# Kernel tuning notes

Hardware: AMD Instinct MI355X
Metric: run time of the kernel (lower is better)

The kernel has to match this reference:

```python
import jax, jax.numpy as jnp
import numpy as np

N_NODES = 20000
NUM_KERNELS = 2
K_DIFF = 10  # max_diffusion_step
IN_DIM = 128
HID = 128
COMB = IN_DIM + HID  # 256
N_EDGES = 640000


def setup_inputs() -> dict:
    key = jax.random.key(0)
    ks = jax.random.split(key, 6)
    inp = jax.random.normal(ks[0], (N_NODES, IN_DIM), dtype=jnp.float32)
    hidden = jax.random.normal(ks[1], (N_NODES, HID), dtype=jnp.float32)
    edge_index = jax.random.randint(ks[2], (NUM_KERNELS, 2, N_EDGES), 0, N_NODES, dtype=jnp.int32)
    # ~row-stochastic-ish weights (avg degree 32) to keep diffusion stable
    edge_weight = jax.random.uniform(ks[3], (NUM_KERNELS, N_EDGES), dtype=jnp.float32) * (1.0 / 32.0)
    num_matrices = NUM_KERNELS * K_DIFF + 1  # 21
    W = jax.random.normal(ks[4], (num_matrices * COMB, HID), dtype=jnp.float32) * (1.0 / np.sqrt(num_matrices * COMB))
    b = jnp.zeros((HID,), dtype=jnp.float32)
    return {"input": inp, "hidden": hidden, "edge_index": edge_index,
            "edge_weight": edge_weight, "W": W, "b": b}


def _gconv(x, edge_index, edge_weight, W, b):
    # x: (N, F). Diffusion (Chebyshev) over each sparse support, concat, project.
    n = x.shape[0]
    feats = [x]  # x_0 shared across kernels
    for k in range(NUM_KERNELS):
        src = edge_index[k, 0]
        dst = edge_index[k, 1]
        w = edge_weight[k][:, None]

        def spmm(v):  # (A v)[dst] = sum_e w_e * v[src_e]
            return jax.ops.segment_sum(v[src] * w, dst, num_segments=n)

        x0, x1 = x, spmm(x)
        feats.append(x1)
        for _ in range(2, K_DIFF + 1):
            x2 = 2.0 * spmm(x1) - x0
            feats.append(x2)
            x0, x1 = x1, x2
    h = jnp.concatenate(feats, axis=1)  # (N, (NUM_KERNELS*K+1)*F)
    return h @ W + b


def reference(input, hidden, edge_index, edge_weight, W, b):
    combined = jnp.concatenate([input, hidden], axis=1)  # (N, COMB)
    r = jax.nn.sigmoid(_gconv(combined, edge_index, edge_weight, W, b))
    u = jax.nn.sigmoid(_gconv(combined, edge_index, edge_weight, W, b))
    combined2 = jnp.concatenate([input, r * hidden], axis=1)
    C = jax.nn.sigmoid(_gconv(combined2, edge_index, edge_weight, W, b))  # activation=sigmoid (default)
    output = u * hidden + (1.0 - u) * C
    return output  # output == new hidden
```

## Files before the change

kernel.cpp:

```cpp
#include <hip/hip_runtime.h>

#define NN 20000
#define NK 2
#define FC 256
#define FH 128
#define NE 640000
#define NB 21

typedef short v8s __attribute__((ext_vector_type(8)));
typedef float v4f __attribute__((ext_vector_type(4)));
typedef unsigned int uint;
typedef uint v2u __attribute__((ext_vector_type(2)));

__device__ __forceinline__ float bf2f(unsigned short h) {
    union { uint u; float f; } v; v.u = ((uint)h) << 16; return v.f;
}
__device__ __forceinline__ unsigned short f2bf(float f) {
    union { float f; uint u; } v; v.f = f;
    uint r = v.u + 0x7FFF + ((v.u >> 16) & 1);
    return (unsigned short)(r >> 16);
}
__device__ __forceinline__ float bflo(uint v) {
    union { uint u; float f; } t; t.u = v << 16; return t.f;
}
__device__ __forceinline__ float bfhi(uint v) {
    union { uint u; float f; } t; t.u = v & 0xffff0000u; return t.f;
}


__global__ __launch_bounds__(256) void k_hist(const int* __restrict__ ei, int* __restrict__ cnt) {
    int wg = blockIdx.x;
    int xcd = wg & 7, chunk = wg >> 3;
    int k = xcd & 1, q = xcd >> 1;
    int e = chunk * 256 + threadIdx.x;
    int dst = ei[(size_t)k * 2 * NE + NE + e];
    if (dst >= q * 5000 && dst < q * 5000 + 5000)
        atomicAdd(&cnt[k * NN + dst], 1);
}

__global__ __launch_bounds__(1024) void k_scan(const int* __restrict__ cnt, int* __restrict__ rp) {
    int k = blockIdx.x;
    __shared__ int part[1024];
    int t = threadIdx.x;
    int loc[20];
    int s = 0;
    if (t < 1000) {
#pragma unroll
        for (int j = 0; j < 20; ++j) { loc[j] = cnt[k * NN + t * 20 + j]; s += loc[j]; }
    }
    part[t] = s;
    __syncthreads();
    for (int off = 1; off < 1024; off <<= 1) {
        int add = (t >= off) ? part[t - off] : 0;
        __syncthreads();
        part[t] += add;
        __syncthreads();
    }
    int excl = (t == 0) ? 0 : part[t - 1];
    if (t < 1000) {
        int run = excl;
#pragma unroll
        for (int j = 0; j < 20; ++j) { rp[k * (NN + 1) + t * 20 + j] = run; run += loc[j]; }
        if (t == 999) rp[k * (NN + 1) + NN] = run;
    }
}

__global__ __launch_bounds__(256) void k_fill(const int* __restrict__ ei, const float* __restrict__ ew,
                                              const int* __restrict__ rp, int* __restrict__ fcnt,
                                              int2* __restrict__ ep) {
    int wg = blockIdx.x;
    int xcd = wg & 7, chunk = wg >> 3;
    int k = xcd & 1, q = xcd >> 1;
    int e = chunk * 256 + threadIdx.x;
    int dst = ei[(size_t)k * 2 * NE + NE + e];
    if (dst >= q * 5000 && dst < q * 5000 + 5000) {
        int src = ei[(size_t)k * 2 * NE + e];
        int pos = rp[k * (NN + 1) + dst] + atomicAdd(&fcnt[k * NN + dst], 1);
        int2 pk; pk.x = src; pk.y = __float_as_int(ew[(size_t)k * NE + e]);
        ep[(size_t)k * NE + pos] = pk;
    }
}


__global__ __launch_bounds__(256) void k_comb(const float* __restrict__ in, const float* __restrict__ hid,
                                              unsigned short* __restrict__ comb) {
    int i = blockIdx.x * 256 + threadIdx.x;
    int r = i >> 6, c4 = i & 63;
    float4 v = (c4 < 32) ? ((const float4*)(in  + (size_t)r * FH))[c4]
                         : ((const float4*)(hid + (size_t)r * FH))[c4 - 32];
    ushort4 o; o.x = f2bf(v.x); o.y = f2bf(v.y); o.z = f2bf(v.z); o.w = f2bf(v.w);
    *(ushort4*)&comb[(size_t)r * FC + c4 * 4] = o;
}


__global__ __launch_bounds__(256) void k_wcvt(const float* __restrict__ W, unsigned short* __restrict__ Wt) {
    int i = blockIdx.x * 256 + threadIdx.x;
    int blk = i >> 15;
    int rem = i & 32767;
    int n = rem >> 8, kk = rem & 255;
    Wt[i] = f2bf(W[((size_t)blk * FC + kk) * FH + n]);
}


#define LDK 72

__global__ __launch_bounds__(256, 2) void k_gemm(const unsigned short* __restrict__ X,
        const unsigned short* __restrict__ Wt, unsigned short* __restrict__ outb,
        float* __restrict__ outf, int jstep) {
    __shared__ unsigned short Xs[64 * LDK];
    __shared__ unsigned short Ws[128 * LDK];
    int t = threadIdx.x;
    int w = t >> 6, l = t & 63;
    int l15 = l & 15, lg = l >> 4;
    int bm = blockIdx.x * 64;
    int blk = jstep + 10 * blockIdx.y;
    const unsigned short* Wb = Wt + (size_t)blk * FH * FC;
    v4f acc[4][2];
#pragma unroll
    for (int a = 0; a < 4; ++a)
#pragma unroll
        for (int b = 0; b < 2; ++b) acc[a][b] = (v4f){0.f, 0.f, 0.f, 0.f};

    for (int c = 0; c < 4; ++c) {
#pragma unroll
        for (int i = 0; i < 2; ++i) {
            int s = t + i * 256;
            int row = s >> 3, c8 = s & 7;
            int grow = bm + row; if (grow >= NN) grow = NN - 1;
            *(v8s*)&Xs[row * LDK + c8 * 8] = *(const v8s*)(X + (size_t)grow * FC + c * 64 + c8 * 8);
        }
#pragma unroll
        for (int i = 0; i < 4; ++i) {
            int s = t + i * 256;
            int n = s >> 3, k8 = s & 7;
            *(v8s*)&Ws[n * LDK + k8 * 8] = *(const v8s*)(Wb + (size_t)n * FC + c * 64 + k8 * 8);
        }
        __syncthreads();
#pragma unroll
        for (int ks2 = 0; ks2 < 2; ++ks2) {
            int ko = ks2 * 32 + lg * 8;
            v8s a[4], b[2];
#pragma unroll
            for (int mf = 0; mf < 4; ++mf) a[mf] = *(const v8s*)&Xs[(mf * 16 + l15) * LDK + ko];
#pragma unroll
            for (int nf = 0; nf < 2; ++nf) b[nf] = *(const v8s*)&Ws[(w * 32 + nf * 16 + l15) * LDK + ko];
#pragma unroll
            for (int mf = 0; mf < 4; ++mf)
#pragma unroll
                for (int nf = 0; nf < 2; ++nf)
                    acc[mf][nf] = __builtin_amdgcn_mfma_f32_16x16x32_bf16(a[mf], b[nf], acc[mf][nf], 0, 0, 0);
        }
        __syncthreads();
    }
    unsigned short* ob = outb ? outb + (size_t)blockIdx.y * NN * FH : (unsigned short*)0;
#pragma unroll
    for (int mf = 0; mf < 4; ++mf) {
        int grow0 = bm + mf * 16 + lg * 4;
#pragma unroll
        for (int nf = 0; nf < 2; ++nf) {
            int gcol = w * 32 + nf * 16 + l15;
#pragma unroll
            for (int r = 0; r < 4; ++r) {
                int grow = grow0 + r;
                if (grow < NN) {
                    if (outf) outf[(size_t)grow * FH + gcol] = acc[mf][nf][r];
                    else      ob[(size_t)grow * FH + gcol] = f2bf(acc[mf][nf][r]);
                }
            }
        }
    }
}


__global__ __launch_bounds__(256) void k_spmm(const int* __restrict__ rp, const int2* __restrict__ ep,
        const v2u* __restrict__ b1, const v2u* __restrict__ b2,
        const v2u* __restrict__ y, v2u* __restrict__ outp, int mode) {
    int wg = blockIdx.x;
    int xcd = wg & 7, slot = wg >> 3;
    int k = (xcd >= 4) ? 1 : 0;
    int unit = (xcd & 3) * 1250 + slot;
    int lane = threadIdx.x & 63;
    int l31 = lane & 31, hl = lane >> 5;
    int row = unit * 4 + (threadIdx.x >> 6);
    int beg = rp[k * (NN + 1) + row], end = rp[k * (NN + 1) + row + 1];
    const v2u* __restrict__ gb = b1 + (size_t)k * NN * 32;
    const long long* epk = (const long long*)(ep + (size_t)k * NE);

    float a0 = 0.f, a1 = 0.f, a2 = 0.f, a3 = 0.f;

    for (int e0 = beg; e0 < end; e0 += 64) {
        int idx = e0 + lane;
        long long mye = (idx < end) ? __builtin_nontemporal_load(epk + idx) : 0ll;
        int mx = (int)mye;
        int my = (int)(mye >> 32);
        int cnt = min(64, end - e0);
        int j = 0;
        for (; j < cnt; j += 16) {
            v2u v[8]; float wv[8];
#pragma unroll
            for (int p = 0; p < 8; ++p) {
                int sA = __builtin_amdgcn_readlane(mx, j + 2 * p);
                int sB = __builtin_amdgcn_readlane(mx, j + 2 * p + 1);
                int s = hl ? sB : sA;
                v[p] = gb[(size_t)s * 32 + l31];
                int wA = __builtin_amdgcn_readlane(my, j + 2 * p);
                int wB = __builtin_amdgcn_readlane(my, j + 2 * p + 1);
                wv[p] = __int_as_float(hl ? wB : wA);
            }
#pragma unroll
            for (int p = 0; p < 8; ++p) {
                a0 += wv[p] * bflo(v[p].x); a1 += wv[p] * bfhi(v[p].x);
                a2 += wv[p] * bflo(v[p].y); a3 += wv[p] * bfhi(v[p].y);
            }
        }
    }
    a0 += __shfl_xor(a0, 32);
    a1 += __shfl_xor(a1, 32);
    a2 += __shfl_xor(a2, 32);
    a3 += __shfl_xor(a3, 32);

    if (hl == 0) {
        size_t o = (size_t)(k * NN + row) * 32 + l31;
        float r0, r1, r2, r3;
        if (mode == 0) {
            v2u yv = __builtin_nontemporal_load(y + o);
            r0 = bflo(yv.x) + 2.f * a0; r1 = bfhi(yv.x) + 2.f * a1;
            r2 = bflo(yv.y) + 2.f * a2; r3 = bfhi(yv.y) + 2.f * a3;
        } else if (mode == 1) {
            v2u yv = __builtin_nontemporal_load(y + o);
            v2u bv = __builtin_nontemporal_load(b2 + o);
            r0 = bflo(yv.x) + 2.f * a0 - bflo(bv.x); r1 = bfhi(yv.x) + 2.f * a1 - bfhi(bv.x);
            r2 = bflo(yv.y) + 2.f * a2 - bflo(bv.y); r3 = bfhi(yv.y) + 2.f * a3 - bfhi(bv.y);
        } else {
            v2u bv = __builtin_nontemporal_load(b2 + o);
            r0 = a0 - bflo(bv.x); r1 = a1 - bfhi(bv.x);
            r2 = a2 - bflo(bv.y); r3 = a3 - bfhi(bv.y);
        }
        v2u res;
        res.x = (uint)f2bf(r0) | ((uint)f2bf(r1) << 16);
        res.y = (uint)f2bf(r2) | ((uint)f2bf(r3) << 16);
        __builtin_nontemporal_store(res, outp + o);
    }
}


__global__ __launch_bounds__(256) void k_act(const float* __restrict__ S0, const unsigned short* __restrict__ Sk,
        const float* __restrict__ bvec, const float* __restrict__ hid,
        float* __restrict__ rbuf, unsigned short* __restrict__ comb) {
    int i = blockIdx.x * 256 + threadIdx.x;
    int r = i >> 7, c = i & 127;
    float s = S0[i] + bf2f(Sk[i]) + bf2f(Sk[(size_t)NN * FH + i]) + bvec[c];
    float u = 1.f / (1.f + __expf(-s));
    rbuf[i] = u;
    comb[(size_t)r * FC + FH + c] = f2bf(u * hid[i]);
}

__global__ __launch_bounds__(256) void k_final(const float* __restrict__ S0, const unsigned short* __restrict__ Sk,
        const float* __restrict__ bvec, const float* __restrict__ hid,
        const float* __restrict__ rbuf, float* __restrict__ out) {
    int i = blockIdx.x * 256 + threadIdx.x;
    int c = i & 127;
    float s = S0[i] + bf2f(Sk[i]) + bf2f(Sk[(size_t)NN * FH + i]) + bvec[c];
    float C = 1.f / (1.f + __expf(-s));
    float u = rbuf[i];
    out[i] = u * hid[i] + (1.f - u) * C;
}


extern "C" void kernel_launch(void* const* d_in, const int* in_sizes, int n_in,
                              void* d_out, int out_size, void* d_ws, size_t ws_size,
                              hipStream_t stream) {
    const float* inp = (const float*)d_in[0];
    const float* hid = (const float*)d_in[1];
    const int*   ei  = (const int*)d_in[2];
    const float* ew  = (const float*)d_in[3];
    const float* W   = (const float*)d_in[4];
    const float* bv  = (const float*)d_in[5];
    float* out = (float*)d_out;

    char* base = (char*)d_ws;
    size_t off = 0;
    auto carve = [&](size_t bytes) -> char* {
        char* q = base + off;
        off += (bytes + 255) & ~(size_t)255;
        return q;
    };
    int*            cnt  = (int*)carve((size_t)2 * NN * 4);
    int*            fcnt = (int*)carve((size_t)2 * NN * 4);
    int*            rp   = (int*)carve((size_t)2 * (NN + 1) * 4);
    int2*           ep   = (int2*)carve((size_t)2 * NE * 8);
    unsigned short* comb = (unsigned short*)carve((size_t)NN * FC * 2);
    unsigned short* Wt   = (unsigned short*)carve((size_t)NB * FH * FC * 2);
    unsigned short* ytmp = (unsigned short*)carve((size_t)2 * NN * FH * 2);
    unsigned short* Bs0  = (unsigned short*)carve((size_t)2 * NN * FH * 2);
    unsigned short* Bs1  = (unsigned short*)carve((size_t)2 * NN * FH * 2);
    unsigned short* Bs2  = (unsigned short*)carve((size_t)2 * NN * FH * 2);
    float*          Sacc = (float*)carve((size_t)NN * FH * 4);
    float*          rbuf = (float*)carve((size_t)NN * FH * 4);
    unsigned short* Bsl[3] = {Bs0, Bs1, Bs2};

    hipMemsetAsync(cnt, 0, (size_t)2 * NN * 4, stream);
    hipMemsetAsync(fcnt, 0, (size_t)2 * NN * 4, stream);
    k_hist<<<20000, 256, 0, stream>>>(ei, cnt);
    k_scan<<<2, 1024, 0, stream>>>(cnt, rp);
    k_fill<<<20000, 256, 0, stream>>>(ei, ew, rp, fcnt, ep);
    k_comb<<<5000, 256, 0, stream>>>(inp, hid, comb);
    k_wcvt<<<2688, 256, 0, stream>>>(W, Wt);

    auto gemm = [&](int j, unsigned short* ob, float* of, int gy) {
        k_gemm<<<dim3(313, gy), 256, 0, stream>>>(comb, Wt, ob, of, j);
    };
    auto spmm = [&](unsigned short* b1, unsigned short* b2, unsigned short* y,
                    unsigned short* o, int mode) {
        k_spmm<<<10000, 256, 0, stream>>>(rp, ep, (const v2u*)b1, (const v2u*)b2,
                                          (const v2u*)y, (v2u*)o, mode);
    };

    auto gconv = [&]() -> unsigned short* {
        gemm(0, nullptr, Sacc, 1);
        gemm(10, Bsl[0], nullptr, 2);
        gemm(9, ytmp, nullptr, 2);
        spmm(Bsl[0], nullptr, ytmp, Bsl[1], 0);
        int cur = 1, prev = 0;
        for (int j = 8; j >= 1; --j) {
            int nxt = 3 - cur - prev;
            gemm(j, ytmp, nullptr, 2);
            spmm(Bsl[cur], Bsl[prev], ytmp, Bsl[nxt], 1);
            prev = cur; cur = nxt;
        }
        int fr = 3 - cur - prev;
        spmm(Bsl[cur], Bsl[prev], nullptr, Bsl[fr], 2);
        return Bsl[fr];
    };

    unsigned short* S1 = gconv();
    k_act<<<10000, 256, 0, stream>>>(Sacc, S1, bv, hid, rbuf, comb);
    unsigned short* S2 = gconv();
    k_final<<<10000, 256, 0, stream>>>(Sacc, S2, bv, hid, rbuf, out);
}
```

Measured before the change: 1.146 ms.

## Split SpMM feature columns into two halves for L2-resident gathers

The GEMM output buffers are re-laid out as two 64-column halves per kernel, and the SpMM grid doubles so each workgroup gathers only a 128-byte half-row slice. Each XCD then works on a smaller working set of the gathered matrix, meant to raise L2 hit rate on the random neighbour gathers. The cost is twice as many workgroups, each re-reading the edge list, plus narrower 4-byte loads per lane. The change also switches edge-index loads to nontemporal and drops nontemporal hints on some SpMM loads and stores.

```diff
diff --git a/kernel.cpp b/kernel.cpp
--- a/kernel.cpp
+++ b/kernel.cpp
@@ -10,7 +10,6 @@
 typedef short v8s __attribute__((ext_vector_type(8)));
 typedef float v4f __attribute__((ext_vector_type(4)));
 typedef unsigned int uint;
-typedef uint v2u __attribute__((ext_vector_type(2)));
 
 __device__ __forceinline__ float bf2f(unsigned short h) {
     union { uint u; float f; } v; v.u = ((uint)h) << 16; return v.f;
@@ -33,7 +32,7 @@
     int xcd = wg & 7, chunk = wg >> 3;
     int k = xcd & 1, q = xcd >> 1;
     int e = chunk * 256 + threadIdx.x;
-    int dst = ei[(size_t)k * 2 * NE + NE + e];
+    int dst = __builtin_nontemporal_load(ei + (size_t)k * 2 * NE + NE + e);
     if (dst >= q * 5000 && dst < q * 5000 + 5000)
         atomicAdd(&cnt[k * NN + dst], 1);
 }
@@ -72,11 +71,12 @@
     int xcd = wg & 7, chunk = wg >> 3;
     int k = xcd & 1, q = xcd >> 1;
     int e = chunk * 256 + threadIdx.x;
-    int dst = ei[(size_t)k * 2 * NE + NE + e];
+    int dst = __builtin_nontemporal_load(ei + (size_t)k * 2 * NE + NE + e);
     if (dst >= q * 5000 && dst < q * 5000 + 5000) {
-        int src = ei[(size_t)k * 2 * NE + e];
+        int src = __builtin_nontemporal_load(ei + (size_t)k * 2 * NE + e);
+        float w = __builtin_nontemporal_load(ew + (size_t)k * NE + e);
         int pos = rp[k * (NN + 1) + dst] + atomicAdd(&fcnt[k * NN + dst], 1);
-        int2 pk; pk.x = src; pk.y = __float_as_int(ew[(size_t)k * NE + e]);
+        int2 pk; pk.x = src; pk.y = __float_as_int(w);
         ep[(size_t)k * NE + pos] = pk;
     }
 }
@@ -159,12 +159,13 @@
 #pragma unroll
         for (int nf = 0; nf < 2; ++nf) {
             int gcol = w * 32 + nf * 16 + l15;
+            int hh = gcol >> 6, c63 = gcol & 63;
 #pragma unroll
             for (int r = 0; r < 4; ++r) {
                 int grow = grow0 + r;
                 if (grow < NN) {
                     if (outf) outf[(size_t)grow * FH + gcol] = acc[mf][nf][r];
-                    else      ob[(size_t)grow * FH + gcol] = f2bf(acc[mf][nf][r]);
+                    else      ob[((size_t)hh * NN + grow) * 64 + c63] = f2bf(acc[mf][nf][r]);
                 }
             }
         }
@@ -173,17 +174,16 @@
 
 
 __global__ __launch_bounds__(256) void k_spmm(const int* __restrict__ rp, const int2* __restrict__ ep,
-        const v2u* __restrict__ b1, const v2u* __restrict__ b2,
-        const v2u* __restrict__ y, v2u* __restrict__ outp, int mode) {
+        const uint* __restrict__ b1, const uint* __restrict__ b2,
+        const uint* __restrict__ y, uint* __restrict__ outp, int mode) {
     int wg = blockIdx.x;
-    int xcd = wg & 7, slot = wg >> 3;
-    int k = (xcd >= 4) ? 1 : 0;
-    int unit = (xcd & 3) * 1250 + slot;
+    int g = wg & 7, slot = wg >> 3;
+    int k = g >> 2, h = (g >> 1) & 1, rh = g & 1;
     int lane = threadIdx.x & 63;
     int l31 = lane & 31, hl = lane >> 5;
-    int row = unit * 4 + (threadIdx.x >> 6);
+    int row = (rh * 2500 + slot) * 4 + (threadIdx.x >> 6);
     int beg = rp[k * (NN + 1) + row], end = rp[k * (NN + 1) + row + 1];
-    const v2u* __restrict__ gb = b1 + (size_t)k * NN * 32;
+    const uint* __restrict__ gb = b1 + (size_t)(k * 2 + h) * NN * 32;
     const long long* epk = (const long long*)(ep + (size_t)k * NE);
 
     float a0 = 0.f, a1 = 0.f, a2 = 0.f, a3 = 0.f;
@@ -194,52 +194,44 @@
         int mx = (int)mye;
         int my = (int)(mye >> 32);
         int cnt = min(64, end - e0);
-        int j = 0;
-        for (; j < cnt; j += 16) {
-            v2u v[8]; float wv[8];
+        for (int j = 0; j < cnt; j += 16) {
+            uint v[8]; float wv[8];
 #pragma unroll
             for (int p = 0; p < 8; ++p) {
                 int sA = __builtin_amdgcn_readlane(mx, j + 2 * p);
                 int sB = __builtin_amdgcn_readlane(mx, j + 2 * p + 1);
                 int s = hl ? sB : sA;
-                v[p] = gb[(size_t)s * 32 + l31];
+                v[p] = gb[(uint)(s * 32 + l31)];
                 int wA = __builtin_amdgcn_readlane(my, j + 2 * p);
                 int wB = __builtin_amdgcn_readlane(my, j + 2 * p + 1);
                 wv[p] = __int_as_float(hl ? wB : wA);
             }
 #pragma unroll
-            for (int p = 0; p < 8; ++p) {
-                a0 += wv[p] * bflo(v[p].x); a1 += wv[p] * bfhi(v[p].x);
-                a2 += wv[p] * bflo(v[p].y); a3 += wv[p] * bfhi(v[p].y);
+            for (int p = 0; p < 8; p += 2) {
+                a0 += wv[p] * bflo(v[p]);         a1 += wv[p] * bfhi(v[p]);
+                a2 += wv[p + 1] * bflo(v[p + 1]); a3 += wv[p + 1] * bfhi(v[p + 1]);
             }
         }
     }
+    a0 += a2; a1 += a3;
     a0 += __shfl_xor(a0, 32);
     a1 += __shfl_xor(a1, 32);
-    a2 += __shfl_xor(a2, 32);
-    a3 += __shfl_xor(a3, 32);
 
     if (hl == 0) {
-        size_t o = (size_t)(k * NN + row) * 32 + l31;
-        float r0, r1, r2, r3;
+        size_t o = ((size_t)(k * 2 + h) * NN + row) * 32 + l31;
+        float r0, r1;
         if (mode == 0) {
-            v2u yv = __builtin_nontemporal_load(y + o);
-            r0 = bflo(yv.x) + 2.f * a0; r1 = bfhi(yv.x) + 2.f * a1;
-            r2 = bflo(yv.y) + 2.f * a2; r3 = bfhi(yv.y) + 2.f * a3;
+            uint yv = __builtin_nontemporal_load(y + o);
+            r0 = bflo(yv) + 2.f * a0; r1 = bfhi(yv) + 2.f * a1;
         } else if (mode == 1) {
-            v2u yv = __builtin_nontemporal_load(y + o);
-            v2u bv = __builtin_nontemporal_load(b2 + o);
-            r0 = bflo(yv.x) + 2.f * a0 - bflo(bv.x); r1 = bfhi(yv.x) + 2.f * a1 - bfhi(bv.x);
-            r2 = bflo(yv.y) + 2.f * a2 - bflo(bv.y); r3 = bfhi(yv.y) + 2.f * a3 - bfhi(bv.y);
+            uint yv = __builtin_nontemporal_load(y + o);
+            uint bv = b2[o];
+            r0 = bflo(yv) + 2.f * a0 - bflo(bv); r1 = bfhi(yv) + 2.f * a1 - bfhi(bv);
         } else {
-            v2u bv = __builtin_nontemporal_load(b2 + o);
-            r0 = a0 - bflo(bv.x); r1 = a1 - bfhi(bv.x);
-            r2 = a2 - bflo(bv.y); r3 = a3 - bfhi(bv.y);
-        }
-        v2u res;
-        res.x = (uint)f2bf(r0) | ((uint)f2bf(r1) << 16);
-        res.y = (uint)f2bf(r2) | ((uint)f2bf(r3) << 16);
-        __builtin_nontemporal_store(res, outp + o);
+            uint bv = b2[o];
+            r0 = a0 - bflo(bv); r1 = a1 - bfhi(bv);
+        }
+        outp[o] = (uint)f2bf(r0) | ((uint)f2bf(r1) << 16);
     }
 }
 
@@ -249,7 +241,9 @@
         float* __restrict__ rbuf, unsigned short* __restrict__ comb) {
     int i = blockIdx.x * 256 + threadIdx.x;
     int r = i >> 7, c = i & 127;
-    float s = S0[i] + bf2f(Sk[i]) + bf2f(Sk[(size_t)NN * FH + i]) + bvec[c];
+    int h = c >> 6, c63 = c & 63;
+    float s = S0[i] + bf2f(Sk[((size_t)h * NN + r) * 64 + c63])
+                    + bf2f(Sk[((size_t)(2 + h) * NN + r) * 64 + c63]) + bvec[c];
     float u = 1.f / (1.f + __expf(-s));
     rbuf[i] = u;
     comb[(size_t)r * FC + FH + c] = f2bf(u * hid[i]);
@@ -259,8 +253,10 @@
         const float* __restrict__ bvec, const float* __restrict__ hid,
         const float* __restrict__ rbuf, float* __restrict__ out) {
     int i = blockIdx.x * 256 + threadIdx.x;
-    int c = i & 127;
-    float s = S0[i] + bf2f(Sk[i]) + bf2f(Sk[(size_t)NN * FH + i]) + bvec[c];
+    int r = i >> 7, c = i & 127;
+    int h = c >> 6, c63 = c & 63;
+    float s = S0[i] + bf2f(Sk[((size_t)h * NN + r) * 64 + c63])
+                    + bf2f(Sk[((size_t)(2 + h) * NN + r) * 64 + c63]) + bvec[c];
     float C = 1.f / (1.f + __expf(-s));
     float u = rbuf[i];
     out[i] = u * hid[i] + (1.f - u) * C;
@@ -312,8 +308,8 @@
     };
     auto spmm = [&](unsigned short* b1, unsigned short* b2, unsigned short* y,
                     unsigned short* o, int mode) {
-        k_spmm<<<10000, 256, 0, stream>>>(rp, ep, (const v2u*)b1, (const v2u*)b2,
-                                          (const v2u*)y, (v2u*)o, mode);
+        k_spmm<<<20000, 256, 0, stream>>>(rp, ep, (const uint*)b1, (const uint*)b2,
+                                          (const uint*)y, (uint*)o, mode);
     };
 
     auto gconv = [&]() -> unsigned short* {
```

New measurement: 1.554 ms. 35.6% more time.
